# Optimization experiments

Hardware: AMD Instinct MI355X
Metric: run time of the kernel (lower is better)

The kernel has to match this reference:

```python
import jax, jax.numpy as jnp
import numpy as np

CHUNK = 64  # mamba chunk size


def _ssd_chunk_scan(x, dt, A, Bs, Cs, R):
    """Exact chunked selective scan (mamba_chunk_scan_combined math, no D skip).
    x: [B,L,H,P] (H=K*R heads), dt: [B,L,H] (already softplus'd),
    A: [H], Bs/Cs: [B,L,K,N] groups (head h uses group h//R).
    Returns y: [B,L,H,P]."""
    Bsz, L, Hh, P = x.shape
    K, N = Bs.shape[2], Bs.shape[3]
    Nc = L // CHUNK
    # broadcast groups -> heads (head k*R+r uses group k)
    Bh = jnp.repeat(Bs, R, axis=2)  # [B,L,H,N]
    Ch = jnp.repeat(Cs, R, axis=2)
    xc = x.reshape(Bsz, Nc, CHUNK, Hh, P)
    dtc = dt.reshape(Bsz, Nc, CHUNK, Hh)
    Bc = Bh.reshape(Bsz, Nc, CHUNK, Hh, N)
    Cc = Ch.reshape(Bsz, Nc, CHUNK, Hh, N)
    dA = jnp.transpose(dtc, (0, 1, 3, 2)) * A[None, None, :, None]  # [B,Nc,H,Q]
    Acum = jnp.cumsum(dA, axis=-1)
    # intra-chunk decay matrix Lmat[i,j] = exp(sum_{j<s<=i} dA_s), lower-tri
    diff = Acum[..., :, None] - Acum[..., None, :]  # [B,Nc,H,Q,Q]
    tri = jnp.tril(jnp.ones((CHUNK, CHUNK), bool))
    Lmat = jnp.where(tri, jnp.exp(diff), 0.0)
    xdt = xc * dtc[..., None]  # dt enters as dt_j * B_j * x_j
    Y_diag = jnp.einsum('bcqhn,bcshn,bchqs,bcshp->bcqhp', Cc, Bc, Lmat, xdt)
    # chunk end states
    decay_last = jnp.exp(Acum[..., -1:] - Acum)  # [B,Nc,H,Q]
    states = jnp.einsum('bcqhn,bchq,bcqhp->bchpn', Bc, decay_last, xdt)
    chunk_decay = jnp.exp(Acum[..., -1])  # [B,Nc,H]
    def step(S, inp):
        cd, st = inp
        return cd[..., None, None] * S + st, S  # emit state BEFORE this chunk
    S0 = jnp.zeros((Bsz, Hh, P, N), x.dtype)
    _, prev = jax.lax.scan(step, S0, (jnp.moveaxis(chunk_decay, 1, 0), jnp.moveaxis(states, 1, 0)))
    prev = jnp.moveaxis(prev, 0, 1)  # [B,Nc,H,P,N]
    Y_off = jnp.einsum('bcqhn,bchpn,bchq->bcqhp', Cc, prev, jnp.exp(Acum))
    return (Y_diag + Y_off).reshape(Bsz, L, Hh, P)


def _forward(x, in_proj_w, conv_w, conv_b, x_proj_w, A_logs, Ds, dt_bias,
             out_norm_g, out_norm_b, out_proj_w):
    B, H, W, Dm = x.shape
    K, R = A_logs.shape
    P = Ds.shape[2]               # headdim
    d_inner = x_proj_w.shape[2]
    N = (x_proj_w.shape[1] - R) // 2
    L = H * W
    # in_proj + gate split
    xz = jnp.einsum('bhwc,dc->bhwd', x, in_proj_w)
    xi, z = jnp.split(xz, 2, axis=-1)
    z = jax.nn.gelu(z, approximate=False)
    # depthwise 3x3 conv (torch weight [d_inner,1,3,3] -> HWIO [3,3,1,d_inner])
    kern = jnp.transpose(conv_w, (2, 3, 1, 0))
    xi = jax.lax.conv_general_dilated(xi, kern, (1, 1), 'SAME',
            dimension_numbers=('NHWC', 'HWIO', 'NHWC'),
            feature_group_count=d_inner) + conv_b
    xi = jax.nn.gelu(xi, approximate=False)
    # cross2d scan: row-major, col-major, and their reverses
    x0 = xi.reshape(B, L, d_inner)
    x1 = jnp.transpose(xi, (0, 2, 1, 3)).reshape(B, L, d_inner)
    xs = jnp.stack([x0, x1, x0[:, ::-1], x1[:, ::-1]], axis=2)  # [B,L,K,d_inner]
    x_dbl = jnp.einsum('blkd,kcd->blkc', xs, x_proj_w)
    dts = x_dbl[..., :R].reshape(B, L, K * R)
    Bs = x_dbl[..., R:R + N]
    Cs = x_dbl[..., R + N:]
    xs_h = xs.reshape(B, L, K * R, P)
    A = -jnp.exp(A_logs.astype(jnp.float32)).reshape(K * R)
    Dmat = Ds.astype(jnp.float32).reshape(K * R, P)
    dt = jax.nn.softplus(dts + dt_bias.reshape(K * R))
    ys = _ssd_chunk_scan(xs_h, dt, A, Bs, Cs, R) + xs_h * Dmat  # D skip on raw x
    ys = ys.reshape(B, L, K, d_inner)
    # cross merge: invert each scan order, sum over K
    def unT(y):
        return jnp.transpose(y.reshape(B, W, H, d_inner), (0, 2, 1, 3)).reshape(B, L, d_inner)
    y = ys[:, :, 0] + ys[:, ::-1, 2] + unT(ys[:, :, 1]) + unT(ys[:, ::-1, 3])
    # out LayerNorm
    y = y.reshape(B, H, W, d_inner)
    mu = y.mean(-1, keepdims=True)
    var = y.var(-1, keepdims=True)
    y = (y - mu) / jnp.sqrt(var + 1e-5) * out_norm_g + out_norm_b
    y = y * z  # gating
    return jnp.einsum('bhwd,cd->bhwc', y, out_proj_w)


def setup_inputs() -> dict:
    key = jax.random.key(0)
    ks = jax.random.split(key, 10)
    B, H, W, Dm = 2, 64, 64, 192
    d_inner, K, R, N = 384, 4, 12, 64
    P = d_inner // R  # 32
    s = 0.02
    return {
        'x': jax.random.normal(ks[0], (B, H, W, Dm), jnp.float32),
        'in_proj_w': s * jax.random.normal(ks[1], (2 * d_inner, Dm), jnp.float32),
        'conv_w': s * jax.random.normal(ks[2], (d_inner, 1, 3, 3), jnp.float32),
        'conv_b': s * jax.random.normal(ks[3], (d_inner,), jnp.float32),
        'x_proj_w': s * jax.random.normal(ks[4], (K, R + 2 * N, d_inner), jnp.float32),
        'A_logs': 0.5 * jax.random.normal(ks[5], (K, R), jnp.float32),
        'Ds': jax.random.uniform(ks[6], (K, R, P), jnp.float32),
        'dt_bias': 0.1 * jax.random.uniform(ks[7], (K, R), jnp.float32),
        'out_norm_g': jnp.ones((d_inner,), jnp.float32),
        'out_norm_b': jnp.zeros((d_inner,), jnp.float32),
        'out_proj_w': s * jax.random.normal(ks[8], (Dm, d_inner), jnp.float32),
    }


def reference(x, in_proj_w, conv_w, conv_b, x_proj_w, A_logs, Ds, dt_bias,
              out_norm_g, out_norm_b, out_proj_w):
    return _forward(x, in_proj_w, conv_w, conv_b, x_proj_w, A_logs, Ds, dt_bias,
                    out_norm_g, out_norm_b, out_proj_w)
```

## Files before the change

kernel.cpp:

```cpp
#include <hip/hip_runtime.h>
#include <math.h>

#define DI 384

typedef __attribute__((ext_vector_type(8))) short bf8v;
typedef __attribute__((ext_vector_type(4))) float f4v;

__device__ __forceinline__ f4v mfma16(bf8v a, bf8v b, f4v c) {
  return __builtin_amdgcn_mfma_f32_16x16x32_bf16(a, b, c, 0, 0, 0);
}

__device__ __forceinline__ int trf(int l) { return ((l & 63) << 6) | (l >> 6); }
__device__ __forceinline__ int mapk(int k, int l) {
  if (k == 0) return l;
  if (k == 1) return trf(l);
  if (k == 2) return 4095 - l;
  return trf(4095 - l);
}
__device__ __forceinline__ float gelu_f(float x) {
  return 0.5f * x * (1.0f + erff(x * 0.7071067811865475f));
}
__device__ __forceinline__ float softplus_f(float x) {
  return (x > 20.0f) ? x : log1pf(expf(x));
}
__device__ __forceinline__ unsigned short f2bf(float f) {
  unsigned u = __float_as_uint(f);
  unsigned r = (u + 0x7fff + ((u >> 16) & 1)) >> 16;
  return (unsigned short)r;
}
__device__ __forceinline__ float bf2f(unsigned short h) {
  return __uint_as_float(((unsigned)h) << 16);
}
__device__ __forceinline__ int swz(int row, int col) {
  return (row << 6) + ((((col >> 3) ^ (row & 7)) << 3) | (col & 7));
}
__device__ __forceinline__ int foff(int row, int cb) {
  return (row << 6) + ((cb ^ (row & 7)) << 3);
}

__global__ __launch_bounds__(256) void k_cvt(const float* __restrict__ src,
                                             unsigned short* __restrict__ hi,
                                             unsigned short* __restrict__ lo, int n) {
  int i = blockIdx.x * 256 + threadIdx.x;
  if (i >= n) return;
  float v = src[i];
  unsigned short h = f2bf(v);
  hi[i] = h;
  lo[i] = f2bf(v - bf2f(h));
}

__global__ __launch_bounds__(256) void k_inproj(const unsigned short* __restrict__ Ahi,
                                                const unsigned short* __restrict__ Alo,
                                                const unsigned short* __restrict__ Whi,
                                                const unsigned short* __restrict__ Wlo,
                                                float* __restrict__ xi_raw,
                                                float* __restrict__ zg) {
  const int K = 192;
  __shared__ unsigned short Ah[4096], Al[4096], Bh[4096], Bl[4096];
  int tid = threadIdx.x;
  int lane = tid & 63, w = tid >> 6;
  int cl = lane & 15, kb = lane >> 4;
  int wm = w >> 1, wn = w & 1;
  int m0 = blockIdx.y * 64, n0 = blockIdx.x * 64;
  f4v acc[2][2];
  acc[0][0] = acc[0][1] = acc[1][0] = acc[1][1] = (f4v){0.f, 0.f, 0.f, 0.f};
  for (int k0 = 0; k0 < K; k0 += 64) {
#pragma unroll
    for (int u = 0; u < 2; ++u) {
      int unit = tid + u * 256;
      int row = unit >> 3, blk = unit & 7;
      int e = foff(row, blk);
      size_t ga = (size_t)(m0 + row) * K + k0 + blk * 8;
      size_t gb = (size_t)(n0 + row) * K + k0 + blk * 8;
      *(bf8v*)(Ah + e) = *(const bf8v*)(Ahi + ga);
      *(bf8v*)(Al + e) = *(const bf8v*)(Alo + ga);
      *(bf8v*)(Bh + e) = *(const bf8v*)(Whi + gb);
      *(bf8v*)(Bl + e) = *(const bf8v*)(Wlo + gb);
    }
    __syncthreads();
#pragma unroll
    for (int chunk = 0; chunk < 2; ++chunk) {
      int cb = chunk * 4 + kb;
      bf8v ah[2], al[2], bh[2], bl[2];
#pragma unroll
      for (int mi = 0; mi < 2; ++mi) {
        ah[mi] = *(const bf8v*)(Ah + foff(wm * 32 + mi * 16 + cl, cb));
        al[mi] = *(const bf8v*)(Al + foff(wm * 32 + mi * 16 + cl, cb));
      }
#pragma unroll
      for (int ni = 0; ni < 2; ++ni) {
        bh[ni] = *(const bf8v*)(Bh + foff(wn * 32 + ni * 16 + cl, cb));
        bl[ni] = *(const bf8v*)(Bl + foff(wn * 32 + ni * 16 + cl, cb));
      }
#pragma unroll
      for (int mi = 0; mi < 2; ++mi)
#pragma unroll
        for (int ni = 0; ni < 2; ++ni) {
          acc[mi][ni] = mfma16(ah[mi], bh[ni], acc[mi][ni]);
          acc[mi][ni] = mfma16(ah[mi], bl[ni], acc[mi][ni]);
          acc[mi][ni] = mfma16(al[mi], bh[ni], acc[mi][ni]);
        }
    }
    __syncthreads();
  }
#pragma unroll
  for (int mi = 0; mi < 2; ++mi)
#pragma unroll
    for (int ni = 0; ni < 2; ++ni)
#pragma unroll
      for (int i = 0; i < 4; ++i) {
        int m = m0 + wm * 32 + mi * 16 + kb * 4 + i;
        int n = n0 + wn * 32 + ni * 16 + cl;
        float v = acc[mi][ni][i];
        if (n < DI) xi_raw[(size_t)m * DI + n] = v;
        else zg[(size_t)m * DI + (n - DI)] = gelu_f(v);
      }
}

__global__ __launch_bounds__(256) void k_conv(const float* __restrict__ xin,
                                              const float* __restrict__ cw,
                                              const float* __restrict__ cb,
                                              unsigned short* __restrict__ xhi,
                                              unsigned short* __restrict__ xlo,
                                              unsigned short* __restrict__ xthi,
                                              unsigned short* __restrict__ xtlo) {
  int idx = blockIdx.x * 256 + threadIdx.x;
  int c = idx % DI;
  int lf = idx / DI;
  int b = lf >> 12;
  int l = lf & 4095;
  int h = l >> 6, w = l & 63;
  float acc = cb[c];
#pragma unroll
  for (int dh = -1; dh <= 1; ++dh) {
    int hh = h + dh;
    if ((unsigned)hh >= 64u) continue;
#pragma unroll
    for (int dw = -1; dw <= 1; ++dw) {
      int ww = w + dw;
      if ((unsigned)ww >= 64u) continue;
      acc += xin[((size_t)((b << 12) | (hh << 6) | ww)) * DI + c] *
             cw[c * 9 + (dh + 1) * 3 + (dw + 1)];
    }
  }
  float g = gelu_f(acc);
  unsigned short hv = f2bf(g);
  unsigned short lv = f2bf(g - bf2f(hv));
  xhi[(size_t)idx] = hv;
  xlo[(size_t)idx] = lv;
  size_t tof = ((size_t)((b << 12) | trf(l))) * DI + c;
  xthi[tof] = hv;
  xtlo[tof] = lv;
}

__global__ __launch_bounds__(256) void k_xproj(const unsigned short* __restrict__ xhi,
                                               const unsigned short* __restrict__ xlo,
                                               const unsigned short* __restrict__ Whi,
                                               const unsigned short* __restrict__ Wlo,
                                               const float* __restrict__ dt_bias,
                                               float* __restrict__ dt_buf,
                                               unsigned short* __restrict__ Bhi,
                                               unsigned short* __restrict__ Blo,
                                               unsigned short* __restrict__ Chi,
                                               unsigned short* __restrict__ Clo) {
  const int K = DI, N = 140;
  int kdir = blockIdx.z;
  __shared__ unsigned short Ah[4096], Al[4096], Bh[4096], Bl[4096];
  __shared__ int rowbase[64];
  int tid = threadIdx.x;
  int lane = tid & 63, w = tid >> 6;
  int cl = lane & 15, kb = lane >> 4;
  int wm = w >> 1, wn = w & 1;
  int m0 = blockIdx.y * 64, n0 = blockIdx.x * 64;
  if (tid < 64) {
    int m = m0 + tid;
    int b = m >> 12, l = m & 4095;
    rowbase[tid] = (b << 12) + mapk(kdir, l);
  }
  const unsigned short* wkh = Whi + (size_t)kdir * N * K;
  const unsigned short* wkl = Wlo + (size_t)kdir * N * K;
  f4v acc[2][2];
  acc[0][0] = acc[0][1] = acc[1][0] = acc[1][1] = (f4v){0.f, 0.f, 0.f, 0.f};
  __syncthreads();
  for (int k0 = 0; k0 < K; k0 += 64) {
#pragma unroll
    for (int u = 0; u < 2; ++u) {
      int unit = tid + u * 256;
      int row = unit >> 3, blk = unit & 7;
      int e = foff(row, blk);
      size_t ga = (size_t)rowbase[row] * K + k0 + blk * 8;
      *(bf8v*)(Ah + e) = *(const bf8v*)(xhi + ga);
      *(bf8v*)(Al + e) = *(const bf8v*)(xlo + ga);
      int n = n0 + row;
      if (n < N) {
        size_t gb = (size_t)n * K + k0 + blk * 8;
        *(bf8v*)(Bh + e) = *(const bf8v*)(wkh + gb);
        *(bf8v*)(Bl + e) = *(const bf8v*)(wkl + gb);
      } else {
        bf8v z = {0, 0, 0, 0, 0, 0, 0, 0};
        *(bf8v*)(Bh + e) = z;
        *(bf8v*)(Bl + e) = z;
      }
    }
    __syncthreads();
#pragma unroll
    for (int chunk = 0; chunk < 2; ++chunk) {
      int cb = chunk * 4 + kb;
      bf8v ah[2], al[2], bh[2], bl[2];
#pragma unroll
      for (int mi = 0; mi < 2; ++mi) {
        ah[mi] = *(const bf8v*)(Ah + foff(wm * 32 + mi * 16 + cl, cb));
        al[mi] = *(const bf8v*)(Al + foff(wm * 32 + mi * 16 + cl, cb));
      }
#pragma unroll
      for (int ni = 0; ni < 2; ++ni) {
        bh[ni] = *(const bf8v*)(Bh + foff(wn * 32 + ni * 16 + cl, cb));
        bl[ni] = *(const bf8v*)(Bl + foff(wn * 32 + ni * 16 + cl, cb));
      }
#pragma unroll
      for (int mi = 0; mi < 2; ++mi)
#pragma unroll
        for (int ni = 0; ni < 2; ++ni) {
          acc[mi][ni] = mfma16(ah[mi], bh[ni], acc[mi][ni]);
          acc[mi][ni] = mfma16(ah[mi], bl[ni], acc[mi][ni]);
          acc[mi][ni] = mfma16(al[mi], bh[ni], acc[mi][ni]);
        }
    }
    __syncthreads();
  }
#pragma unroll
  for (int mi = 0; mi < 2; ++mi)
#pragma unroll
    for (int ni = 0; ni < 2; ++ni)
#pragma unroll
      for (int i = 0; i < 4; ++i) {
        int m = m0 + wm * 32 + mi * 16 + kb * 4 + i;
        int n = n0 + wn * 32 + ni * 16 + cl;
        if (n >= N) continue;
        float v = acc[mi][ni][i];
        int b = m >> 12, l = m & 4095;
        if (n < 12) {
          dt_buf[(((size_t)(b * 48 + kdir * 12 + n)) << 12) + l] =
              softplus_f(v + dt_bias[kdir * 12 + n]);
        } else if (n < 76) {
          size_t off = (((size_t)((b * 4 + kdir) << 12)) + l) * 64 + (n - 12);
          unsigned short hh = f2bf(v);
          Bhi[off] = hh;
          Blo[off] = f2bf(v - bf2f(hh));
        } else {
          size_t off = (((size_t)((b * 4 + kdir) << 12)) + l) * 64 + (n - 76);
          unsigned short hh = f2bf(v);
          Chi[off] = hh;
          Clo[off] = f2bf(v - bf2f(hh));
        }
      }
}

__global__ __launch_bounds__(256) void k_dtacum(const float* __restrict__ dt_buf,
                                                const float* __restrict__ A_logs,
                                                float* __restrict__ ac_buf,
                                                float* __restrict__ cdec) {
  int bh = blockIdx.y;
  int c = blockIdx.x * 4 + (threadIdx.x >> 6);
  int lane = threadIdx.x & 63;
  int h = bh % 48;
  size_t o = ((size_t)bh << 12) + c * 64 + lane;
  float dtv = dt_buf[o];
  float v = dtv * (-__expf(A_logs[h]));
#pragma unroll
  for (int off = 1; off < 64; off <<= 1) {
    float u = __shfl_up(v, off, 64);
    if (lane >= off) v += u;
  }
  ac_buf[o] = v;
  if (lane == 63) cdec[bh * 64 + c] = __expf(v);
}

__global__ __launch_bounds__(256) void k_states(const unsigned short* __restrict__ xhi,
                                                const unsigned short* __restrict__ xthi,
                                                const float* __restrict__ dt_buf,
                                                const float* __restrict__ ac_buf,
                                                const unsigned short* __restrict__ Bhi,
                                                unsigned short* __restrict__ Shi) {
  int c = blockIdx.x, k = blockIdx.y >> 1, g = blockIdx.y & 1, b = blockIdx.z;
  __shared__ unsigned short Bt_h[4096];
  __shared__ unsigned short xw_h[2048];
  int tid = threadIdx.x;
  int lane = tid & 63, w = tid >> 6;
  int cl = lane & 15, kb = lane >> 4;
  size_t Bbase = (((size_t)((b * 4 + k) << 12)) + c * 64) * 64;
  {
    int n = lane;
#pragma unroll
    for (int it = 0; it < 8; ++it) {
      int q0 = 2 * (w + it * 4);
      unsigned short h0 = Bhi[Bbase + (size_t)q0 * 64 + n];
      unsigned short h1 = Bhi[Bbase + (size_t)(q0 + 1) * 64 + n];
      *(unsigned int*)(Bt_h + swz(n, q0)) = (unsigned)h0 | ((unsigned)h1 << 16);
    }
  }
  const unsigned short* xp = (k & 1) ? xthi : xhi;
  int p_s = tid & 31, qg = tid >> 5;
  for (int rr = 0; rr < 6; ++rr) {
    int r = g * 6 + rr;
    int h = k * 12 + r;
    unsigned short rh0[4], rh1[4];
#pragma unroll
    for (int it = 0; it < 4; ++it) {
      int q0 = 2 * (qg + it * 8);
      int i0 = c * 64 + q0, i1 = i0 + 1;
      if (k & 2) { i0 = 4095 - i0; i1 = 4094 - (i1 - 1) - 1 + 0; i1 = 4095 - (c * 64 + q0 + 1); }
      rh0[it] = xp[((size_t)((b << 12) + i0)) * DI + r * 32 + p_s];
      rh1[it] = xp[((size_t)((b << 12) + i1)) * DI + r * 32 + p_s];
    }
    size_t dto = (((size_t)(b * 48 + h)) << 12) + c * 64 + lane;
    float dtv = dt_buf[dto];
    float v = ac_buf[dto];
    float alast = __shfl(v, 63, 64);
    float wq = dtv * __expf(alast - v);
    __syncthreads();
#pragma unroll
    for (int it = 0; it < 4; ++it) {
      int q0 = 2 * (qg + it * 8);
      float w0 = __shfl(wq, q0, 64), w1 = __shfl(wq, q0 + 1, 64);
      unsigned short h0 = f2bf(bf2f(rh0[it]) * w0);
      unsigned short h1 = f2bf(bf2f(rh1[it]) * w1);
      *(unsigned int*)(xw_h + swz(p_s, q0)) = (unsigned)h0 | ((unsigned)h1 << 16);
    }
    __syncthreads();
    f4v acc0 = {0.f, 0.f, 0.f, 0.f}, acc1 = {0.f, 0.f, 0.f, 0.f};
#pragma unroll
    for (int chunk = 0; chunk < 2; ++chunk) {
      int cb_ = chunk * 4 + kb;
      bf8v bh = *(const bf8v*)(Bt_h + foff(w * 16 + cl, cb_));
      bf8v a0h = *(const bf8v*)(xw_h + foff(cl, cb_));
      bf8v a1h = *(const bf8v*)(xw_h + foff(16 + cl, cb_));
      acc0 = mfma16(a0h, bh, acc0);
      acc1 = mfma16(a1h, bh, acc1);
    }
    size_t sbase = ((size_t)(b * 48 + h) * 64 + c) * 2048;
#pragma unroll
    for (int i = 0; i < 4; ++i) {
      int prow = kb * 4 + i;
      int n = w * 16 + cl;
      Shi[sbase + (size_t)prow * 64 + n] = f2bf(acc0[i]);
      Shi[sbase + (size_t)(16 + prow) * 64 + n] = f2bf(acc1[i]);
    }
  }
}

__global__ __launch_bounds__(256) void k_scan(unsigned short* __restrict__ Shi,
                                              const float* __restrict__ cdec) {
  int j = blockIdx.x;
  int bh = blockIdx.y;
  int tid = threadIdx.x;
  size_t base0 = (size_t)bh * 64 * 2048 + j * 256 + tid;
  float S = 0.0f;
  float nxt = bf2f(Shi[base0]);
  for (int c = 0; c < 64; ++c) {
    float cd = cdec[bh * 64 + c];
    size_t idx = base0 + (size_t)c * 2048;
    float tmp = nxt;
    if (c < 63) nxt = bf2f(Shi[idx + 2048]);
    Shi[idx] = f2bf(S);
    S = cd * S + tmp;
  }
}

__global__ __launch_bounds__(256) void k_out(const unsigned short* __restrict__ xhi,
                                             const unsigned short* __restrict__ xlo,
                                             const unsigned short* __restrict__ xthi,
                                             const unsigned short* __restrict__ xtlo,
                                             const float* __restrict__ dt_buf,
                                             const float* __restrict__ ac_buf,
                                             const unsigned short* __restrict__ Bhi,
                                             const unsigned short* __restrict__ Blo,
                                             const unsigned short* __restrict__ Chi,
                                             const unsigned short* __restrict__ Clo,
                                             const float* __restrict__ Ds,
                                             const unsigned short* __restrict__ Phi,
                                             float* __restrict__ ys) {
  int c = blockIdx.x, k = blockIdx.y >> 1, g = blockIdx.y & 1, b = blockIdx.z;
  __shared__ unsigned short C_h[4096], C_l[4096];
  __shared__ unsigned short G_h[4096];
  __shared__ unsigned short Xbuf[4096];
  unsigned short* X_h = Xbuf;
  unsigned short* X_l = Xbuf + 2048;
  int tid = threadIdx.x;
  int lane = tid & 63, w = tid >> 6;
  int cl = lane & 15, kb = lane >> 4;
  size_t base64 = (((size_t)((b * 4 + k) << 12)) + c * 64) * 64;
  {
    int n0 = (tid & 31) * 2;
    int qq = tid >> 5;
#pragma unroll
    for (int it = 0; it < 8; ++it) {
      int q = qq + it * 8;
      size_t off = base64 + (size_t)q * 64 + n0;
      int e = swz(q, n0);
      *(unsigned int*)(C_h + e) = *(const unsigned int*)(Chi + off);
      *(unsigned int*)(C_l + e) = *(const unsigned int*)(Clo + off);
      *(unsigned int*)(G_h + e) = *(const unsigned int*)(Bhi + off);
      *(unsigned int*)(Xbuf + e) = *(const unsigned int*)(Blo + off);
    }
  }
  __syncthreads();
  bf8v caf_h[2], caf_l[2];
#pragma unroll
  for (int chunk = 0; chunk < 2; ++chunk) {
    caf_h[chunk] = *(const bf8v*)(C_h + foff(w * 16 + cl, chunk * 4 + kb));
    caf_l[chunk] = *(const bf8v*)(C_l + foff(w * 16 + cl, chunk * 4 + kb));
  }
  f4v cbt[4];
#pragma unroll
  for (int St = 0; St < 4; ++St) cbt[St] = (f4v){0.f, 0.f, 0.f, 0.f};
#pragma unroll
  for (int St = 0; St < 4; ++St) {
    int srow = St * 16 + cl;
#pragma unroll
    for (int chunk = 0; chunk < 2; ++chunk) {
      bf8v bh = *(const bf8v*)(G_h + foff(srow, chunk * 4 + kb));
      bf8v bl = *(const bf8v*)(Xbuf + foff(srow, chunk * 4 + kb));
      cbt[St] = mfma16(caf_h[chunk], bh, cbt[St]);
      cbt[St] = mfma16(caf_h[chunk], bl, cbt[St]);
      cbt[St] = mfma16(caf_l[chunk], bh, cbt[St]);
    }
  }
  const unsigned short* xph = (k & 1) ? xthi : xhi;
  const unsigned short* xpl = (k & 1) ? xtlo : xlo;
  int p_s = tid & 31, sg = tid >> 5;
  int h0_ = k * 12 + g * 6;
  bf8v pfA[2][2], pfB[2][2];
  {
    size_t pb = ((size_t)(b * 48 + h0_) * 64 + c) * 2048;
#pragma unroll
    for (int chunk = 0; chunk < 2; ++chunk) {
      int cb_ = chunk * 4 + kb;
      pfA[chunk][0] = *(const bf8v*)(Phi + pb + (size_t)cl * 64 + cb_ * 8);
      pfA[chunk][1] = *(const bf8v*)(Phi + pb + (size_t)(16 + cl) * 64 + cb_ * 8);
    }
  }
  size_t dto0 = (((size_t)(b * 48 + h0_)) << 12) + c * 64 + lane;
  float dtA = dt_buf[dto0];
  float vA = ac_buf[dto0];
  float dtB, vB;
  for (int rr = 0; rr < 6; ++rr) {
    int r = g * 6 + rr;
    int h = k * 12 + r;
    float dtv = dtA;
    float v = vA;
    float ea = __expf(v);
    __syncthreads();
#pragma unroll
    for (int it = 0; it < 4; ++it) {
      int s0 = 2 * (sg + it * 8);
      int i0 = c * 64 + s0, i1 = i0 + 1;
      if (k & 2) { i0 = 4095 - i0; i1 = i0 - 1; }
      size_t o0 = ((size_t)((b << 12) + i0)) * DI + r * 32 + p_s;
      size_t o1 = ((size_t)((b << 12) + i1)) * DI + r * 32 + p_s;
      int e = swz(p_s, s0);
      *(unsigned int*)(X_h + e) = (unsigned)xph[o0] | ((unsigned)xph[o1] << 16);
      *(unsigned int*)(X_l + e) = (unsigned)xpl[o0] | ((unsigned)xpl[o1] << 16);
    }
    float vq[4];
#pragma unroll
    for (int i = 0; i < 4; ++i) vq[i] = __shfl(v, w * 16 + kb * 4 + i, 64);
#pragma unroll
    for (int St = 0; St < 4; ++St) {
      int s = St * 16 + cl;
      float vs = __shfl(v, s, 64);
      float dts = __shfl(dtv, s, 64);
#pragma unroll
      for (int i = 0; i < 4; ++i) {
        int q = w * 16 + kb * 4 + i;
        float gv = (q >= s) ? cbt[St][i] * __expf(vq[i] - vs) * dts : 0.0f;
        G_h[swz(q, s)] = f2bf(gv);
      }
    }
    __syncthreads();
    if (rr < 5) {
      size_t pbn = ((size_t)(b * 48 + h + 1) * 64 + c) * 2048;
#pragma unroll
      for (int chunk = 0; chunk < 2; ++chunk) {
        int cb_ = chunk * 4 + kb;
        pfB[chunk][0] = *(const bf8v*)(Phi + pbn + (size_t)cl * 64 + cb_ * 8);
        pfB[chunk][1] = *(const bf8v*)(Phi + pbn + (size_t)(16 + cl) * 64 + cb_ * 8);
      }
      size_t dton = (((size_t)(b * 48 + h + 1)) << 12) + c * 64 + lane;
      dtB = dt_buf[dton];
      vB = ac_buf[dton];
    }
    f4v aD0 = {0.f, 0.f, 0.f, 0.f}, aD1 = aD0, aO0 = aD0, aO1 = aD0;
#pragma unroll
    for (int chunk = 0; chunk < 2; ++chunk) {
      int cb_ = chunk * 4 + kb;
      int qrow = w * 16 + cl;
      bf8v gh = *(const bf8v*)(G_h + foff(qrow, cb_));
      bf8v x0h = *(const bf8v*)(X_h + foff(cl, cb_));
      bf8v x0l = *(const bf8v*)(X_l + foff(cl, cb_));
      bf8v x1h = *(const bf8v*)(X_h + foff(16 + cl, cb_));
      bf8v x1l = *(const bf8v*)(X_l + foff(16 + cl, cb_));
      aD0 = mfma16(gh, x0h, aD0);
      aD0 = mfma16(gh, x0l, aD0);
      aD1 = mfma16(gh, x1h, aD1);
      aD1 = mfma16(gh, x1l, aD1);
      aO0 = mfma16(caf_h[chunk], pfA[chunk][0], aO0);
      aO0 = mfma16(caf_l[chunk], pfA[chunk][0], aO0);
      aO1 = mfma16(caf_h[chunk], pfA[chunk][1], aO1);
      aO1 = mfma16(caf_l[chunk], pfA[chunk][1], aO1);
    }
    float D0 = Ds[h * 32 + cl], D1 = Ds[h * 32 + 16 + cl];
    size_t ybase = ((size_t)((b * 4 + k) << 12) + c * 64) * DI + r * 32;
#pragma unroll
    for (int i = 0; i < 4; ++i) {
      int q = w * 16 + kb * 4 + i;
      float eaq = __shfl(ea, q, 64);
      int e0 = swz(cl, q), e1 = swz(16 + cl, q);
      float xv0 = bf2f(X_h[e0]) + bf2f(X_l[e0]);
      float xv1 = bf2f(X_h[e1]) + bf2f(X_l[e1]);
      ys[ybase + (size_t)q * DI + cl] = aD0[i] + eaq * aO0[i] + D0 * xv0;
      ys[ybase + (size_t)q * DI + 16 + cl] = aD1[i] + eaq * aO1[i] + D1 * xv1;
    }
#pragma unroll
    for (int chunk = 0; chunk < 2; ++chunk) {
      pfA[chunk][0] = pfB[chunk][0];
      pfA[chunk][1] = pfB[chunk][1];
    }
    dtA = dtB;
    vA = vB;
  }
}

__global__ __launch_bounds__(128) void k_ln(const float* __restrict__ ys,
                                            const float* __restrict__ zg,
                                            const float* __restrict__ gg,
                                            const float* __restrict__ bb,
                                            unsigned short* __restrict__ y2h,
                                            unsigned short* __restrict__ y2l) {
  int row = blockIdx.x;
  int b = row >> 12, l = row & 4095;
  int l1 = trf(l);
  int l2 = 4095 - l;
  int l3 = 4095 - l1;
  int tid = threadIdx.x;
  float v[3];
  size_t base = ((size_t)(b * 4)) << 12;
#pragma unroll
  for (int j = 0; j < 3; ++j) {
    int d = tid + j * 128;
    v[j] = ys[(base + l) * DI + d] + ys[(base + 4096 + l1) * DI + d] +
           ys[(base + 8192 + l2) * DI + d] + ys[(base + 12288 + l3) * DI + d];
  }
  __shared__ float red[2];
  float s = v[0] + v[1] + v[2];
#pragma unroll
  for (int off = 32; off > 0; off >>= 1) s += __shfl_down(s, off, 64);
  if ((tid & 63) == 0) red[tid >> 6] = s;
  __syncthreads();
  float mu = (red[0] + red[1]) * (1.0f / 384.0f);
  __syncthreads();
  float d2 = 0.0f;
#pragma unroll
  for (int j = 0; j < 3; ++j) {
    float dd = v[j] - mu;
    d2 += dd * dd;
  }
#pragma unroll
  for (int off = 32; off > 0; off >>= 1) d2 += __shfl_down(d2, off, 64);
  if ((tid & 63) == 0) red[tid >> 6] = d2;
  __syncthreads();
  float rstd = rsqrtf((red[0] + red[1]) * (1.0f / 384.0f) + 1e-5f);
#pragma unroll
  for (int j = 0; j < 3; ++j) {
    int d = tid + j * 128;
    float yv = (v[j] - mu) * rstd * gg[d] + bb[d];
    float o = yv * zg[(size_t)row * DI + d];
    unsigned short hh = f2bf(o);
    y2h[(size_t)row * DI + d] = hh;
    y2l[(size_t)row * DI + d] = f2bf(o - bf2f(hh));
  }
}

__global__ __launch_bounds__(256) void k_outproj(const unsigned short* __restrict__ Ahi,
                                                 const unsigned short* __restrict__ Alo,
                                                 const unsigned short* __restrict__ Whi,
                                                 const unsigned short* __restrict__ Wlo,
                                                 float* __restrict__ out) {
  const int K = DI, NO = 192;
  __shared__ unsigned short Ah[4096], Al[4096], Bh[4096], Bl[4096];
  int tid = threadIdx.x;
  int lane = tid & 63, w = tid >> 6;
  int cl = lane & 15, kb = lane >> 4;
  int wm = w >> 1, wn = w & 1;
  int m0 = blockIdx.y * 64, n0 = blockIdx.x * 64;
  f4v acc[2][2];
  acc[0][0] = acc[0][1] = acc[1][0] = acc[1][1] = (f4v){0.f, 0.f, 0.f, 0.f};
  for (int k0 = 0; k0 < K; k0 += 64) {
#pragma unroll
    for (int u = 0; u < 2; ++u) {
      int unit = tid + u * 256;
      int row = unit >> 3, blk = unit & 7;
      int e = foff(row, blk);
      size_t ga = (size_t)(m0 + row) * K + k0 + blk * 8;
      size_t gb = (size_t)(n0 + row) * K + k0 + blk * 8;
      *(bf8v*)(Ah + e) = *(const bf8v*)(Ahi + ga);
      *(bf8v*)(Al + e) = *(const bf8v*)(Alo + ga);
      *(bf8v*)(Bh + e) = *(const bf8v*)(Whi + gb);
      *(bf8v*)(Bl + e) = *(const bf8v*)(Wlo + gb);
    }
    __syncthreads();
#pragma unroll
    for (int chunk = 0; chunk < 2; ++chunk) {
      int cb = chunk * 4 + kb;
      bf8v ah[2], al[2], bh[2], bl[2];
#pragma unroll
      for (int mi = 0; mi < 2; ++mi) {
        ah[mi] = *(const bf8v*)(Ah + foff(wm * 32 + mi * 16 + cl, cb));
        al[mi] = *(const bf8v*)(Al + foff(wm * 32 + mi * 16 + cl, cb));
      }
#pragma unroll
      for (int ni = 0; ni < 2; ++ni) {
        bh[ni] = *(const bf8v*)(Bh + foff(wn * 32 + ni * 16 + cl, cb));
        bl[ni] = *(const bf8v*)(Bl + foff(wn * 32 + ni * 16 + cl, cb));
      }
#pragma unroll
      for (int mi = 0; mi < 2; ++mi)
#pragma unroll
        for (int ni = 0; ni < 2; ++ni) {
          acc[mi][ni] = mfma16(ah[mi], bh[ni], acc[mi][ni]);
          acc[mi][ni] = mfma16(ah[mi], bl[ni], acc[mi][ni]);
          acc[mi][ni] = mfma16(al[mi], bh[ni], acc[mi][ni]);
        }
    }
    __syncthreads();
  }
#pragma unroll
  for (int mi = 0; mi < 2; ++mi)
#pragma unroll
    for (int ni = 0; ni < 2; ++ni)
#pragma unroll
      for (int i = 0; i < 4; ++i) {
        int m = m0 + wm * 32 + mi * 16 + kb * 4 + i;
        int n = n0 + wn * 32 + ni * 16 + cl;
        out[(size_t)m * NO + n] = acc[mi][ni][i];
      }
}

extern "C" void kernel_launch(void* const* d_in, const int* in_sizes, int n_in,
                              void* d_out, int out_size, void* d_ws, size_t ws_size,
                              hipStream_t stream) {
  const float* x = (const float*)d_in[0];
  const float* in_proj_w = (const float*)d_in[1];
  const float* conv_w = (const float*)d_in[2];
  const float* conv_b = (const float*)d_in[3];
  const float* x_proj_w = (const float*)d_in[4];
  const float* A_logs = (const float*)d_in[5];
  const float* Ds = (const float*)d_in[6];
  const float* dt_bias = (const float*)d_in[7];
  const float* out_norm_g = (const float*)d_in[8];
  const float* out_norm_b = (const float*)d_in[9];
  const float* out_proj_w = (const float*)d_in[10];
  float* out = (float*)d_out;

  float* ws = (float*)d_ws;
  float* xi_raw = ws;
  float* zg = xi_raw + 3145728;
  float* dt_buf = zg + 3145728;
  float* ac_buf = dt_buf + 393216;
  float* cdec = ac_buf + 393216;
  float* ys = cdec + 6144;
  unsigned short* u16p = (unsigned short*)(ys + 12582912);
  unsigned short* Shi = u16p;    u16p += 12582912;
  unsigned short* xi_hi = u16p;  u16p += 3145728;
  unsigned short* xi_lo = u16p;  u16p += 3145728;
  unsigned short* x_hi = u16p;   u16p += 1572864;
  unsigned short* x_lo = u16p;   u16p += 1572864;
  unsigned short* xit_lo = u16p; u16p += 3145728;
  unsigned short* win_hi = u16p; u16p += 147456;
  unsigned short* win_lo = u16p; u16p += 147456;
  unsigned short* wxp_hi = u16p; u16p += 215040;
  unsigned short* wxp_lo = u16p; u16p += 215040;
  unsigned short* wout_hi = u16p; u16p += 73728;
  unsigned short* wout_lo = u16p; u16p += 73728;
  unsigned short* Bhi = u16p;    u16p += 2097152;
  unsigned short* Blo = u16p;    u16p += 2097152;
  unsigned short* Chi = u16p;    u16p += 2097152;
  unsigned short* Clo = u16p;    u16p += 2097152;
  unsigned short* xit_hi = x_hi;
  unsigned short* y2h = (unsigned short*)xi_raw;
  unsigned short* y2l = y2h + 3145728;

  k_cvt<<<(1572864 + 255) / 256, 256, 0, stream>>>(x, x_hi, x_lo, 1572864);
  k_cvt<<<(147456 + 255) / 256, 256, 0, stream>>>(in_proj_w, win_hi, win_lo, 147456);
  k_cvt<<<(215040 + 255) / 256, 256, 0, stream>>>(x_proj_w, wxp_hi, wxp_lo, 215040);
  k_cvt<<<(73728 + 255) / 256, 256, 0, stream>>>(out_proj_w, wout_hi, wout_lo, 73728);

  k_inproj<<<dim3(12, 128), 256, 0, stream>>>(x_hi, x_lo, win_hi, win_lo, xi_raw, zg);
  k_conv<<<dim3(12288), 256, 0, stream>>>(xi_raw, conv_w, conv_b, xi_hi, xi_lo,
                                          xit_hi, xit_lo);
  k_xproj<<<dim3(3, 128, 4), 256, 0, stream>>>(xi_hi, xi_lo, wxp_hi, wxp_lo, dt_bias,
                                               dt_buf, Bhi, Blo, Chi, Clo);
  k_dtacum<<<dim3(16, 96), 256, 0, stream>>>(dt_buf, A_logs, ac_buf, cdec);
  k_states<<<dim3(64, 8, 2), 256, 0, stream>>>(xi_hi, xit_hi, dt_buf, ac_buf, Bhi, Shi);
  k_scan<<<dim3(8, 96), 256, 0, stream>>>(Shi, cdec);
  k_out<<<dim3(64, 8, 2), 256, 0, stream>>>(xi_hi, xi_lo, xit_hi, xit_lo, dt_buf,
                                            ac_buf, Bhi, Blo, Chi, Clo, Ds, Shi, ys);
  k_ln<<<dim3(8192), 128, 0, stream>>>(ys, zg, out_norm_g, out_norm_b, y2h, y2l);
  k_outproj<<<dim3(3, 128), 256, 0, stream>>>(y2h, y2l, wout_hi, wout_lo, out);
}
```

Baseline: 198.1 us.

## Vectorize and prefetch x loads in states/out kernels, store xi_raw as bf16 pair

```diff
diff --git a/kernel.cpp b/kernel.cpp
--- a/kernel.cpp
+++ b/kernel.cpp
@@ -30,6 +30,10 @@
 }
 __device__ __forceinline__ float bf2f(unsigned short h) {
   return __uint_as_float(((unsigned)h) << 16);
+}
+__device__ __forceinline__ unsigned short el16(uint2 v, int i) {
+  unsigned w = (i < 2) ? v.x : v.y;
+  return (unsigned short)((i & 1) ? (w >> 16) : (w & 0xffffu));
 }
 __device__ __forceinline__ int swz(int row, int col) {
   return (row << 6) + ((((col >> 3) ^ (row & 7)) << 3) | (col & 7));
@@ -53,7 +57,8 @@
                                                 const unsigned short* __restrict__ Alo,
                                                 const unsigned short* __restrict__ Whi,
                                                 const unsigned short* __restrict__ Wlo,
-                                                float* __restrict__ xi_raw,
+                                                unsigned short* __restrict__ xr_hi,
+                                                unsigned short* __restrict__ xr_lo,
                                                 float* __restrict__ zg) {
   const int K = 192;
   __shared__ unsigned short Ah[4096], Al[4096], Bh[4096], Bl[4096];
@@ -112,12 +117,18 @@
         int m = m0 + wm * 32 + mi * 16 + kb * 4 + i;
         int n = n0 + wn * 32 + ni * 16 + cl;
         float v = acc[mi][ni][i];
-        if (n < DI) xi_raw[(size_t)m * DI + n] = v;
-        else zg[(size_t)m * DI + (n - DI)] = gelu_f(v);
-      }
-}
-
-__global__ __launch_bounds__(256) void k_conv(const float* __restrict__ xin,
+        if (n < DI) {
+          unsigned short hh = f2bf(v);
+          xr_hi[(size_t)m * DI + n] = hh;
+          xr_lo[(size_t)m * DI + n] = f2bf(v - bf2f(hh));
+        } else {
+          zg[(size_t)m * DI + (n - DI)] = gelu_f(v);
+        }
+      }
+}
+
+__global__ __launch_bounds__(256) void k_conv(const unsigned short* __restrict__ xrh,
+                                              const unsigned short* __restrict__ xrl,
                                               const float* __restrict__ cw,
                                               const float* __restrict__ cb,
                                               unsigned short* __restrict__ xhi,
@@ -139,8 +150,8 @@
     for (int dw = -1; dw <= 1; ++dw) {
       int ww = w + dw;
       if ((unsigned)ww >= 64u) continue;
-      acc += xin[((size_t)((b << 12) | (hh << 6) | ww)) * DI + c] *
-             cw[c * 9 + (dh + 1) * 3 + (dw + 1)];
+      size_t o = ((size_t)((b << 12) | (hh << 6) | ww)) * DI + c;
+      acc += (bf2f(xrh[o]) + bf2f(xrl[o])) * cw[c * 9 + (dh + 1) * 3 + (dw + 1)];
     }
   }
   float g = gelu_f(acc);
@@ -276,18 +287,32 @@
   if (lane == 63) cdec[bh * 64 + c] = __expf(v);
 }
 
-__global__ __launch_bounds__(256) void k_states(const unsigned short* __restrict__ xhi,
-                                                const unsigned short* __restrict__ xthi,
-                                                const float* __restrict__ dt_buf,
-                                                const float* __restrict__ ac_buf,
-                                                const unsigned short* __restrict__ Bhi,
-                                                unsigned short* __restrict__ Shi) {
+__global__ __launch_bounds__(256, 4) void k_states(const unsigned short* __restrict__ xhi,
+                                                   const unsigned short* __restrict__ xthi,
+                                                   const float* __restrict__ dt_buf,
+                                                   const float* __restrict__ ac_buf,
+                                                   const unsigned short* __restrict__ Bhi,
+                                                   unsigned short* __restrict__ Shi) {
   int c = blockIdx.x, k = blockIdx.y >> 1, g = blockIdx.y & 1, b = blockIdx.z;
   __shared__ unsigned short Bt_h[4096];
   __shared__ unsigned short xw_h[2048];
   int tid = threadIdx.x;
   int lane = tid & 63, w = tid >> 6;
   int cl = lane & 15, kb = lane >> 4;
+  const unsigned short* xp = (k & 1) ? xthi : xhi;
+  int pg = tid & 7, qq = tid >> 3;
+  int h0_ = k * 12 + g * 6;
+  uint2 xgA[2], xgB[2];
+#pragma unroll
+  for (int qp = 0; qp < 2; ++qp) {
+    int i = c * 64 + qq * 2 + qp;
+    if (k & 2) i = 4095 - i;
+    xgA[qp] = *(const uint2*)(xp + ((size_t)((b << 12) + i)) * DI + h0_ % 12 * 32 + pg * 4);
+  }
+  size_t dto0 = (((size_t)(b * 48 + h0_)) << 12) + c * 64 + lane;
+  float dtA = dt_buf[dto0];
+  float acA = ac_buf[dto0];
+  float dtB, acB;
   size_t Bbase = (((size_t)((b * 4 + k) << 12)) + c * 64) * 64;
   {
     int n = lane;
@@ -299,35 +324,33 @@
       *(unsigned int*)(Bt_h + swz(n, q0)) = (unsigned)h0 | ((unsigned)h1 << 16);
     }
   }
-  const unsigned short* xp = (k & 1) ? xthi : xhi;
-  int p_s = tid & 31, qg = tid >> 5;
   for (int rr = 0; rr < 6; ++rr) {
     int r = g * 6 + rr;
     int h = k * 12 + r;
-    unsigned short rh0[4], rh1[4];
-#pragma unroll
-    for (int it = 0; it < 4; ++it) {
-      int q0 = 2 * (qg + it * 8);
-      int i0 = c * 64 + q0, i1 = i0 + 1;
-      if (k & 2) { i0 = 4095 - i0; i1 = 4094 - (i1 - 1) - 1 + 0; i1 = 4095 - (c * 64 + q0 + 1); }
-      rh0[it] = xp[((size_t)((b << 12) + i0)) * DI + r * 32 + p_s];
-      rh1[it] = xp[((size_t)((b << 12) + i1)) * DI + r * 32 + p_s];
-    }
-    size_t dto = (((size_t)(b * 48 + h)) << 12) + c * 64 + lane;
-    float dtv = dt_buf[dto];
-    float v = ac_buf[dto];
+    float v = acA;
     float alast = __shfl(v, 63, 64);
-    float wq = dtv * __expf(alast - v);
-    __syncthreads();
-#pragma unroll
-    for (int it = 0; it < 4; ++it) {
-      int q0 = 2 * (qg + it * 8);
-      float w0 = __shfl(wq, q0, 64), w1 = __shfl(wq, q0 + 1, 64);
-      unsigned short h0 = f2bf(bf2f(rh0[it]) * w0);
-      unsigned short h1 = f2bf(bf2f(rh1[it]) * w1);
-      *(unsigned int*)(xw_h + swz(p_s, q0)) = (unsigned)h0 | ((unsigned)h1 << 16);
-    }
-    __syncthreads();
+    float wq = dtA * __expf(alast - v);
+    float w0 = __shfl(wq, qq * 2, 64), w1 = __shfl(wq, qq * 2 + 1, 64);
+    __syncthreads();
+#pragma unroll
+    for (int pi = 0; pi < 4; ++pi) {
+      int p = pg * 4 + pi;
+      unsigned short h0 = f2bf(bf2f(el16(xgA[0], pi)) * w0);
+      unsigned short h1 = f2bf(bf2f(el16(xgA[1], pi)) * w1);
+      *(unsigned int*)(xw_h + swz(p, qq * 2)) = (unsigned)h0 | ((unsigned)h1 << 16);
+    }
+    __syncthreads();
+    if (rr < 5) {
+#pragma unroll
+      for (int qp = 0; qp < 2; ++qp) {
+        int i = c * 64 + qq * 2 + qp;
+        if (k & 2) i = 4095 - i;
+        xgB[qp] = *(const uint2*)(xp + ((size_t)((b << 12) + i)) * DI + (r + 1) * 32 + pg * 4);
+      }
+      size_t dton = (((size_t)(b * 48 + h + 1)) << 12) + c * 64 + lane;
+      dtB = dt_buf[dton];
+      acB = ac_buf[dton];
+    }
     f4v acc0 = {0.f, 0.f, 0.f, 0.f}, acc1 = {0.f, 0.f, 0.f, 0.f};
 #pragma unroll
     for (int chunk = 0; chunk < 2; ++chunk) {
@@ -346,6 +369,10 @@
       Shi[sbase + (size_t)prow * 64 + n] = f2bf(acc0[i]);
       Shi[sbase + (size_t)(16 + prow) * 64 + n] = f2bf(acc1[i]);
     }
+    xgA[0] = xgB[0];
+    xgA[1] = xgB[1];
+    dtA = dtB;
+    acA = acB;
   }
 }
 
@@ -367,19 +394,19 @@
   }
 }
 
-__global__ __launch_bounds__(256) void k_out(const unsigned short* __restrict__ xhi,
-                                             const unsigned short* __restrict__ xlo,
-                                             const unsigned short* __restrict__ xthi,
-                                             const unsigned short* __restrict__ xtlo,
-                                             const float* __restrict__ dt_buf,
-                                             const float* __restrict__ ac_buf,
-                                             const unsigned short* __restrict__ Bhi,
-                                             const unsigned short* __restrict__ Blo,
-                                             const unsigned short* __restrict__ Chi,
-                                             const unsigned short* __restrict__ Clo,
-                                             const float* __restrict__ Ds,
-                                             const unsigned short* __restrict__ Phi,
-                                             float* __restrict__ ys) {
+__global__ __launch_bounds__(256, 4) void k_out(const unsigned short* __restrict__ xhi,
+                                                const unsigned short* __restrict__ xlo,
+                                                const unsigned short* __restrict__ xthi,
+                                                const unsigned short* __restrict__ xtlo,
+                                                const float* __restrict__ dt_buf,
+                                                const float* __restrict__ ac_buf,
+                                                const unsigned short* __restrict__ Bhi,
+                                                const unsigned short* __restrict__ Blo,
+                                                const unsigned short* __restrict__ Chi,
+                                                const unsigned short* __restrict__ Clo,
+                                                const float* __restrict__ Ds,
+                                                const unsigned short* __restrict__ Phi,
+                                                float* __restrict__ ys) {
   int c = blockIdx.x, k = blockIdx.y >> 1, g = blockIdx.y & 1, b = blockIdx.z;
   __shared__ unsigned short C_h[4096], C_l[4096];
   __shared__ unsigned short G_h[4096];
@@ -389,6 +416,33 @@
   int tid = threadIdx.x;
   int lane = tid & 63, w = tid >> 6;
   int cl = lane & 15, kb = lane >> 4;
+  const unsigned short* xph = (k & 1) ? xthi : xhi;
+  const unsigned short* xpl = (k & 1) ? xtlo : xlo;
+  int pg = tid & 7, sq = tid >> 3;
+  int h0_ = k * 12 + g * 6;
+  uint2 xghA[2], xglA[2], xghB[2], xglB[2];
+#pragma unroll
+  for (int sp = 0; sp < 2; ++sp) {
+    int i = c * 64 + sq * 2 + sp;
+    if (k & 2) i = 4095 - i;
+    size_t o = ((size_t)((b << 12) + i)) * DI + (g * 6 % 12) * 32 + pg * 4;
+    xghA[sp] = *(const uint2*)(xph + o);
+    xglA[sp] = *(const uint2*)(xpl + o);
+  }
+  bf8v pfA[2][2], pfB[2][2];
+  {
+    size_t pb = ((size_t)(b * 48 + h0_) * 64 + c) * 2048;
+#pragma unroll
+    for (int chunk = 0; chunk < 2; ++chunk) {
+      int cb_ = chunk * 4 + kb;
+      pfA[chunk][0] = *(const bf8v*)(Phi + pb + (size_t)cl * 64 + cb_ * 8);
+      pfA[chunk][1] = *(const bf8v*)(Phi + pb + (size_t)(16 + cl) * 64 + cb_ * 8);
+    }
+  }
+  size_t dto0 = (((size_t)(b * 48 + h0_)) << 12) + c * 64 + lane;
+  float dtA = dt_buf[dto0];
+  float vA = ac_buf[dto0];
+  float dtB, vB;
   size_t base64 = (((size_t)((b * 4 + k) << 12)) + c * 64) * 64;
   {
     int n0 = (tid & 31) * 2;
@@ -426,24 +480,6 @@
       cbt[St] = mfma16(caf_l[chunk], bh, cbt[St]);
     }
   }
-  const unsigned short* xph = (k & 1) ? xthi : xhi;
-  const unsigned short* xpl = (k & 1) ? xtlo : xlo;
-  int p_s = tid & 31, sg = tid >> 5;
-  int h0_ = k * 12 + g * 6;
-  bf8v pfA[2][2], pfB[2][2];
-  {
-    size_t pb = ((size_t)(b * 48 + h0_) * 64 + c) * 2048;
-#pragma unroll
-    for (int chunk = 0; chunk < 2; ++chunk) {
-      int cb_ = chunk * 4 + kb;
-      pfA[chunk][0] = *(const bf8v*)(Phi + pb + (size_t)cl * 64 + cb_ * 8);
-      pfA[chunk][1] = *(const bf8v*)(Phi + pb + (size_t)(16 + cl) * 64 + cb_ * 8);
-    }
-  }
-  size_t dto0 = (((size_t)(b * 48 + h0_)) << 12) + c * 64 + lane;
-  float dtA = dt_buf[dto0];
-  float vA = ac_buf[dto0];
-  float dtB, vB;
   for (int rr = 0; rr < 6; ++rr) {
     int r = g * 6 + rr;
     int h = k * 12 + r;
@@ -452,15 +488,13 @@
     float ea = __expf(v);
     __syncthreads();
 #pragma unroll
-    for (int it = 0; it < 4; ++it) {
-      int s0 = 2 * (sg + it * 8);
-      int i0 = c * 64 + s0, i1 = i0 + 1;
-      if (k & 2) { i0 = 4095 - i0; i1 = i0 - 1; }
-      size_t o0 = ((size_t)((b << 12) + i0)) * DI + r * 32 + p_s;
-      size_t o1 = ((size_t)((b << 12) + i1)) * DI + r * 32 + p_s;
-      int e = swz(p_s, s0);
-      *(unsigned int*)(X_h + e) = (unsigned)xph[o0] | ((unsigned)xph[o1] << 16);
-      *(unsigned int*)(X_l + e) = (unsigned)xpl[o0] | ((unsigned)xpl[o1] << 16);
+    for (int pi = 0; pi < 4; ++pi) {
+      int p = pg * 4 + pi;
+      int e = swz(p, sq * 2);
+      *(unsigned int*)(X_h + e) =
+          (unsigned)el16(xghA[0], pi) | ((unsigned)el16(xghA[1], pi) << 16);
+      *(unsigned int*)(X_l + e) =
+          (unsigned)el16(xglA[0], pi) | ((unsigned)el16(xglA[1], pi) << 16);
     }
     float vq[4];
 #pragma unroll
@@ -479,6 +513,14 @@
     }
     __syncthreads();
     if (rr < 5) {
+#pragma unroll
+      for (int sp = 0; sp < 2; ++sp) {
+        int i = c * 64 + sq * 2 + sp;
+        if (k & 2) i = 4095 - i;
+        size_t o = ((size_t)((b << 12) + i)) * DI + (r + 1) * 32 + pg * 4;
+        xghB[sp] = *(const uint2*)(xph + o);
+        xglB[sp] = *(const uint2*)(xpl + o);
+      }
       size_t pbn = ((size_t)(b * 48 + h + 1) * 64 + c) * 2048;
 #pragma unroll
       for (int chunk = 0; chunk < 2; ++chunk) {
@@ -526,6 +568,8 @@
       pfA[chunk][0] = pfB[chunk][0];
       pfA[chunk][1] = pfB[chunk][1];
     }
+    xghA[0] = xghB[0]; xghA[1] = xghB[1];
+    xglA[0] = xglB[0]; xglA[1] = xglB[1];
     dtA = dtB;
     vA = vB;
   }
@@ -687,7 +731,9 @@
   unsigned short* Chi = u16p;    u16p += 2097152;
   unsigned short* Clo = u16p;    u16p += 2097152;
   unsigned short* xit_hi = x_hi;
-  unsigned short* y2h = (unsigned short*)xi_raw;
+  unsigned short* xr_hi = (unsigned short*)xi_raw;
+  unsigned short* xr_lo = xr_hi + 3145728;
+  unsigned short* y2h = xr_hi;
   unsigned short* y2l = y2h + 3145728;
 
   k_cvt<<<(1572864 + 255) / 256, 256, 0, stream>>>(x, x_hi, x_lo, 1572864);
@@ -695,8 +741,8 @@
   k_cvt<<<(215040 + 255) / 256, 256, 0, stream>>>(x_proj_w, wxp_hi, wxp_lo, 215040);
   k_cvt<<<(73728 + 255) / 256, 256, 0, stream>>>(out_proj_w, wout_hi, wout_lo, 73728);
 
-  k_inproj<<<dim3(12, 128), 256, 0, stream>>>(x_hi, x_lo, win_hi, win_lo, xi_raw, zg);
-  k_conv<<<dim3(12288), 256, 0, stream>>>(xi_raw, conv_w, conv_b, xi_hi, xi_lo,
+  k_inproj<<<dim3(12, 128), 256, 0, stream>>>(x_hi, x_lo, win_hi, win_lo, xr_hi, xr_lo, zg);
+  k_conv<<<dim3(12288), 256, 0, stream>>>(xr_hi, xr_lo, conv_w, conv_b, xi_hi, xi_lo,
                                           xit_hi, xit_lo);
   k_xproj<<<dim3(3, 128, 4), 256, 0, stream>>>(xi_hi, xi_lo, wxp_hi, wxp_lo, dt_bias,
                                                dt_buf, Bhi, Blo, Chi, Clo);
```

New measurement: 225.7 us. 1.14x slower.
